# Optimization experiments

Measured on AMD Instinct MI355X. Metric: run time of the kernel, lower is better.

## Reference

```python
import jax, jax.numpy as jnp
import numpy as np

B, S, Lb, C, CP, H = 64, 4, 64, 32, 16, 4
LN_EPS = 1e-5


def layer_norm(x, g, b):
    mu = jnp.mean(x, axis=-1, keepdims=True)
    var = jnp.mean(jnp.square(x - mu), axis=-1, keepdims=True)
    return (x - mu) * jax.lax.rsqrt(var + LN_EPS) * g + b


def mha(x, w_in, b_in, w_out, b_out, h):
    # torch nn.MultiheadAttention, batch_first, self-attention
    Bx, L, Cx = x.shape
    d = Cx // h
    qkv = x @ w_in.T + b_in                      # (Bx, L, 3C)
    q, k, v = jnp.split(qkv, 3, axis=-1)
    sp = lambda t: t.reshape(Bx, L, h, d).transpose(0, 2, 1, 3)  # (Bx,h,L,d)
    q, k, v = sp(q), sp(k), sp(v)
    scale = 1.0 / jnp.sqrt(jnp.asarray(d, x.dtype))
    attn = jax.nn.softmax(jnp.einsum('bhid,bhjd->bhij', q, k) * scale, axis=-1)
    o = jnp.einsum('bhij,bhjd->bhid', attn, v).transpose(0, 2, 1, 3).reshape(Bx, L, Cx)
    return o @ w_out.T + b_out


def setup_inputs() -> dict:
    key = jax.random.key(0)
    ks = jax.random.split(key, 20)
    g = lambda i, shape, s=0.05: (jax.random.normal(ks[i], shape, dtype=jnp.float32) * s)
    inp = {
        'chip_ctcf': jax.random.normal(ks[0], (B, Lb), dtype=jnp.float32),
        'chip_hac':  jax.random.normal(ks[1], (B, Lb), dtype=jnp.float32),
        'chip_me1':  jax.random.normal(ks[2], (B, Lb), dtype=jnp.float32),
        'chip_me3':  jax.random.normal(ks[3], (B, Lb), dtype=jnp.float32),
        'embed_w': g(4, (C, 1)), 'embed_b': g(5, (C,)),
        'pos_embed': g(6, (1, 1, Lb, C), 0.02),
        'row_in_w': g(7, (3 * C, C)), 'row_in_b': g(8, (3 * C,)),
        'row_out_w': g(9, (C, C)), 'row_out_b': g(10, (C,)),
        'row_ln_g': jnp.ones((C,), jnp.float32), 'row_ln_b': jnp.zeros((C,), jnp.float32),
        'col_in_w': g(11, (3 * C, C)), 'col_in_b': g(12, (3 * C,)),
        'col_out_w': g(13, (C, C)), 'col_out_b': g(14, (C,)),
        'col_ln_g': jnp.ones((C,), jnp.float32), 'col_ln_b': jnp.zeros((C,), jnp.float32),
        'proj_w': g(15, (CP, C * C)), 'proj_b': g(16, (CP,)),
        'pln_g': jnp.ones((CP,), jnp.float32), 'pln_b': jnp.zeros((CP,), jnp.float32),
    }
    return inp


def reference(chip_ctcf, chip_hac, chip_me1, chip_me3,
              embed_w, embed_b, pos_embed,
              row_in_w, row_in_b, row_out_w, row_out_b, row_ln_g, row_ln_b,
              col_in_w, col_in_b, col_out_w, col_out_b, col_ln_g, col_ln_b,
              proj_w, proj_b, pln_g, pln_b):
    Bv = chip_ctcf.shape[0]
    signals = jnp.stack([chip_ctcf, chip_hac, chip_me1, chip_me3], axis=1)  # (B,4,64)
    # Linear(1, C): scalar embed
    msa = signals[..., None] * embed_w[:, 0] + embed_b                      # (B,4,64,C)
    msa = msa + pos_embed
    # row attention over the 64 bins, per track
    x = msa.reshape(Bv * S, Lb, C)
    x = layer_norm(x + mha(x, row_in_w, row_in_b, row_out_w, row_out_b, H), row_ln_g, row_ln_b)
    msa = x.reshape(Bv, S, Lb, C)
    # column attention over the 4 tracks, per bin
    x = msa.transpose(0, 2, 1, 3).reshape(Bv * Lb, S, C)
    x = layer_norm(x + mha(x, col_in_w, col_in_b, col_out_w, col_out_b, H), col_ln_g, col_ln_b)
    msa = x.reshape(Bv, Lb, S, C).transpose(0, 2, 1, 3)                     # (B,4,64,C)
    # outer product of the track-mean (as written in the torch source)
    m = jnp.mean(msa, axis=1)                                               # (B,64,C)
    pair = jnp.einsum('bic,bjd->bijcd', m, m).reshape(Bv, Lb, Lb, C * C)    # (B,64,64,1024)
    nrm = jnp.sqrt(jnp.sum(jnp.square(pair), axis=-1, keepdims=True))
    pair = pair / jnp.maximum(nrm, 1e-6)                                    # F.normalize eps=1e-6
    feat = pair @ proj_w.T + proj_b                                         # (B,64,64,CP)
    feat = layer_norm(feat, pln_g, pln_b)
    feat = feat * jax.nn.sigmoid(feat)                                      # SiLU
    return feat.transpose(0, 3, 1, 2)                                       # (B,CP,64,64)
```

## Files before the change

kernel.cpp:

```cpp
#include <hip/hip_runtime.h>
#include <hip/hip_bf16.h>

#define LN_EPS 1e-5f

__global__ __launch_bounds__(256) void k_row(
    const float* __restrict__ ctcf, const float* __restrict__ hac,
    const float* __restrict__ me1,  const float* __restrict__ me3,
    const float* __restrict__ ew,   const float* __restrict__ eb,
    const float* __restrict__ pe,
    const float* __restrict__ w_in, const float* __restrict__ b_in,
    const float* __restrict__ w_out,const float* __restrict__ b_out,
    const float* __restrict__ ln_g, const float* __restrict__ ln_b,
    float* __restrict__ msaR)
{
    __shared__ float sx[64][33];
    __shared__ float sqkv[64 * 100];
    __shared__ float so[64][33];
    __shared__ float swin[96 * 32];
    __shared__ float swout[32 * 32];
    __shared__ float sbin[96];
    __shared__ float sbout[32], sg[32], sb[32];
    __shared__ float smean[64], srstd[64];

    const int blk = blockIdx.x;
    const int s   = blk & 3;
    const int b   = blk >> 2;
    const int tid = threadIdx.x;

    const float* chip = (s == 0) ? ctcf : (s == 1) ? hac : (s == 2) ? me1 : me3;

    for (int n = tid; n < 96 * 32; n += 256) swin[n] = w_in[n];
    for (int n = tid; n < 32 * 32; n += 256) swout[n] = w_out[n];
    if (tid < 96) sbin[tid] = b_in[tid];
    if (tid < 32) {
        sbout[tid] = b_out[tid];
        sg[tid] = ln_g[tid];
        sb[tid] = ln_b[tid];
    }
    for (int n = tid; n < 2048; n += 256) {
        int l = n >> 5, c = n & 31;
        sx[l][c] = chip[b * 64 + l] * ew[c] + eb[c] + pe[l * 32 + c];
    }
    __syncthreads();

    const int l  = tid & 63;
    const int cg = tid >> 6;

    float xr[32];
#pragma unroll
    for (int c = 0; c < 32; ++c) xr[c] = sx[l][c];

#pragma unroll
    for (int i = 0; i < 24; ++i) {
        int cc = i * 4 + cg;
        const float* wr = &swin[cc * 32];
        float acc = sbin[cc];
#pragma unroll
        for (int c = 0; c < 32; ++c) acc += xr[c] * wr[c];
        sqkv[l * 100 + cc] = acc;
    }
    __syncthreads();

    {
        const int h = cg;
        float q[8];
#pragma unroll
        for (int dd = 0; dd < 8; ++dd) q[dd] = sqkv[l * 100 + h * 8 + dd];
        const float scale = 0.35355339059327373f;
        float mrun = -1e30f, denom = 0.f, acc[8];
#pragma unroll
        for (int dd = 0; dd < 8; ++dd) acc[dd] = 0.f;
        for (int j = 0; j < 64; ++j) {
            const float* kr = &sqkv[j * 100 + 32 + h * 8];
            const float* vr = &sqkv[j * 100 + 64 + h * 8];
            float sc = 0.f;
#pragma unroll
            for (int dd = 0; dd < 8; ++dd) sc += q[dd] * kr[dd];
            sc *= scale;
            float mnew = fmaxf(mrun, sc);
            float corr = __expf(mrun - mnew);
            float w = __expf(sc - mnew);
            denom = denom * corr + w;
#pragma unroll
            for (int dd = 0; dd < 8; ++dd)
                acc[dd] = acc[dd] * corr + w * vr[dd];
            mrun = mnew;
        }
        float inv = 1.f / denom;
#pragma unroll
        for (int dd = 0; dd < 8; ++dd) so[l][h * 8 + dd] = acc[dd] * inv;
    }
    __syncthreads();

    {
        float orow[32];
#pragma unroll
        for (int k = 0; k < 32; ++k) orow[k] = so[l][k];
#pragma unroll
        for (int i = 0; i < 8; ++i) {
            int c = i * 4 + cg;
            const float* wr = &swout[c * 32];
            float acc = sbout[c] + xr[c];
#pragma unroll
            for (int k = 0; k < 32; ++k) acc += orow[k] * wr[k];
            sqkv[l * 100 + c] = acc;
        }
    }
    __syncthreads();

    if (tid < 64) {
        float mu = 0.f;
#pragma unroll
        for (int c = 0; c < 32; ++c) mu += sqkv[tid * 100 + c];
        mu *= (1.f / 32.f);
        float var = 0.f;
#pragma unroll
        for (int c = 0; c < 32; ++c) { float d = sqkv[tid * 100 + c] - mu; var += d * d; }
        var *= (1.f / 32.f);
        smean[tid] = mu;
        srstd[tid] = rsqrtf(var + LN_EPS);
    }
    __syncthreads();

    float* outp = msaR + blk * 2048;
    for (int n = tid; n < 2048; n += 256) {
        int ll = n >> 5, c = n & 31;
        outp[n] = (sqkv[ll * 100 + c] - smean[ll]) * srstd[ll] * sg[c] + sb[c];
    }
}

__global__ __launch_bounds__(256) void k_col(
    const float* __restrict__ msaR,
    const float* __restrict__ w_in, const float* __restrict__ b_in,
    const float* __restrict__ w_out,const float* __restrict__ b_out,
    const float* __restrict__ ln_g, const float* __restrict__ ln_b,
    float* __restrict__ m_out, float* __restrict__ nrm_out)
{
    __shared__ float sx[64][33];
    __shared__ float sqkv[64 * 100];
    __shared__ float so[64][33];
    __shared__ float swi[96 * 32];
    __shared__ float swo[32 * 32];
    __shared__ float sbi[96];
    __shared__ float sbo[32], sg[32], sb[32];
    __shared__ float smean2[64], srstd2[64];
    __shared__ float smv[16][33];

    const int bx = blockIdx.x;
    const int b  = bx >> 2;
    const int l0 = (bx & 3) * 16;
    const int tid = threadIdx.x;

    for (int n = tid; n < 96 * 32; n += 256) swi[n] = w_in[n];
    for (int n = tid; n < 32 * 32; n += 256) swo[n] = w_out[n];
    if (tid < 96) sbi[tid] = b_in[tid];
    if (tid < 32) {
        sbo[tid] = b_out[tid];
        sg[tid] = ln_g[tid];
        sb[tid] = ln_b[tid];
    }
    for (int n = tid; n < 2048; n += 256) {
        int s = n >> 9, lo = (n >> 5) & 15, c = n & 31;
        sx[s * 16 + lo][c] = msaR[((b * 4 + s) * 64 + l0 + lo) * 32 + c];
    }
    __syncthreads();

    const int r  = tid & 63;
    const int sS = r & 3, lo = r >> 2;
    const int cg = tid >> 6;

    float xr[32];
#pragma unroll
    for (int c = 0; c < 32; ++c) xr[c] = sx[sS * 16 + lo][c];

#pragma unroll
    for (int i = 0; i < 24; ++i) {
        int cc = i * 4 + cg;
        const float* wr = &swi[cc * 32];
        float acc = sbi[cc];
#pragma unroll
        for (int c = 0; c < 32; ++c) acc += xr[c] * wr[c];
        sqkv[r * 100 + cc] = acc;
    }
    __syncthreads();

    {
        const int la = tid >> 4, h = (tid >> 2) & 3, ia = tid & 3;
        const float scale = 0.35355339059327373f;
        float q[8];
#pragma unroll
        for (int dd = 0; dd < 8; ++dd) q[dd] = sqkv[(la * 4 + ia) * 100 + h * 8 + dd];
        float sc[4];
        float mx = -1e30f;
#pragma unroll
        for (int jj = 0; jj < 4; ++jj) {
            const float* kr = &sqkv[(la * 4 + jj) * 100 + 32 + h * 8];
            float v = 0.f;
#pragma unroll
            for (int dd = 0; dd < 8; ++dd) v += q[dd] * kr[dd];
            sc[jj] = v * scale;
            mx = fmaxf(mx, sc[jj]);
        }
        float den = 0.f;
#pragma unroll
        for (int jj = 0; jj < 4; ++jj) { sc[jj] = __expf(sc[jj] - mx); den += sc[jj]; }
        float inv = 1.f / den;
#pragma unroll
        for (int dd = 0; dd < 8; ++dd) {
            float a = 0.f;
#pragma unroll
            for (int jj = 0; jj < 4; ++jj)
                a += sc[jj] * sqkv[(la * 4 + jj) * 100 + 64 + h * 8 + dd];
            so[la * 4 + ia][h * 8 + dd] = a * inv;
        }
    }
    __syncthreads();

    {
        float orow[32];
#pragma unroll
        for (int k = 0; k < 32; ++k) orow[k] = so[r][k];
#pragma unroll
        for (int i = 0; i < 8; ++i) {
            int c = i * 4 + cg;
            const float* wr = &swo[c * 32];
            float acc = sbo[c] + xr[c];
#pragma unroll
            for (int k = 0; k < 32; ++k) acc += orow[k] * wr[k];
            sqkv[r * 100 + c] = acc;
        }
    }
    __syncthreads();

    if (tid < 64) {
        float mu = 0.f;
#pragma unroll
        for (int c = 0; c < 32; ++c) mu += sqkv[tid * 100 + c];
        mu *= (1.f / 32.f);
        float var = 0.f;
#pragma unroll
        for (int c = 0; c < 32; ++c) { float d = sqkv[tid * 100 + c] - mu; var += d * d; }
        var *= (1.f / 32.f);
        smean2[tid] = mu;
        srstd2[tid] = rsqrtf(var + LN_EPS);
    }
    __syncthreads();

    for (int pass = 0; pass < 2; ++pass) {
        int idx = pass * 256 + tid;
        int loo = idx >> 5, c = idx & 31;
        float acc = 0.f;
#pragma unroll
        for (int ss = 0; ss < 4; ++ss) {
            int rr = loo * 4 + ss;
            acc += (sqkv[rr * 100 + c] - smean2[rr]) * srstd2[rr];
        }
        float mval = 0.25f * acc * sg[c] + sb[c];
        m_out[(b * 64 + l0 + loo) * 32 + c] = mval;
        smv[loo][c] = mval * mval;
    }
    __syncthreads();

    if (tid < 16) {
        float sum = 0.f;
#pragma unroll
        for (int c = 0; c < 32; ++c) sum += smv[tid][c];
        nrm_out[b * 64 + l0 + tid] = sqrtf(sum);
    }
}

__global__ __launch_bounds__(256) void k_pair(
    const float* __restrict__ m, const float* __restrict__ nrm,
    const float* __restrict__ pw, const float* __restrict__ pb,
    const float* __restrict__ pg, const float* __restrict__ pbeta,
    float* __restrict__ out)
{
    __shared__ float spw[512 * 36];
    __shared__ float sT[16 * 520];
    __shared__ float smj[64][33];
    __shared__ float snj[64];
    __shared__ float sbias[16], sgam[16], sbet[16];

    const int bx = blockIdx.x;
    const int b  = bx >> 2;
    const int i0 = (bx & 3) * 16;
    const int tid = threadIdx.x;

    const float* mb = m + b * 2048;
    for (int n = tid; n < 2048; n += 256) smj[n >> 5][n & 31] = mb[n];
    if (tid < 64) snj[tid] = nrm[b * 64 + tid];
    if (tid < 16) {
        sbias[tid] = pb[tid];
        sgam[tid]  = pg[tid];
        sbet[tid]  = pbeta[tid];
    }
    for (int n = tid; n < 16384; n += 256) {
        int cp = n >> 10, c = (n >> 5) & 31, d = n & 31;
        spw[(cp * 32 + d) * 36 + c] = pw[n];
    }
    __syncthreads();

    {
        const int il = tid >> 4, t16 = tid & 15;
        const int ig = i0 + il;
        float mi[32];
#pragma unroll
        for (int c = 0; c < 32; ++c) mi[c] = smj[ig][c];
#pragma unroll
        for (int p = 0; p < 32; ++p) {
            int rem = p * 16 + t16;
            const float* wr = &spw[rem * 36];
            float acc = 0.f;
#pragma unroll
            for (int c = 0; c < 32; ++c) acc += wr[c] * mi[c];
            sT[il * 520 + rem] = acc;
        }
    }
    __syncthreads();

    const int j  = tid & 63;
    const int ih = tid >> 6;
    float mj[32];
#pragma unroll
    for (int d = 0; d < 32; ++d) mj[d] = smj[j][d];
    const float nj = snj[j];

    for (int q = 0; q < 4; ++q) {
        const int il = ih * 4 + q;
        const int ig = i0 + il;
        const float invn = 1.f / fmaxf(snj[ig] * nj, 1e-6f);
        float f[16];
#pragma unroll
        for (int cp = 0; cp < 16; ++cp) {
            const float* tr = &sT[il * 520 + cp * 32];
            float acc = 0.f;
#pragma unroll
            for (int d = 0; d < 32; ++d) acc += tr[d] * mj[d];
            f[cp] = acc * invn + sbias[cp];
        }
        float mu = 0.f;
#pragma unroll
        for (int cp = 0; cp < 16; ++cp) mu += f[cp];
        mu *= (1.f / 16.f);
        float var = 0.f;
#pragma unroll
        for (int cp = 0; cp < 16; ++cp) { float d = f[cp] - mu; var += d * d; }
        var *= (1.f / 16.f);
        const float rstd = rsqrtf(var + LN_EPS);
#pragma unroll
        for (int cp = 0; cp < 16; ++cp) {
            float v = (f[cp] - mu) * rstd * sgam[cp] + sbet[cp];
            float sl = v / (1.f + __expf(-v));
            out[((b * 16 + cp) * 64 + ig) * 64 + j] = sl;
        }
    }
}

extern "C" void kernel_launch(void* const* d_in, const int* in_sizes, int n_in,
                              void* d_out, int out_size, void* d_ws, size_t ws_size,
                              hipStream_t stream) {
    const float* ctcf  = (const float*)d_in[0];
    const float* hac   = (const float*)d_in[1];
    const float* me1   = (const float*)d_in[2];
    const float* me3   = (const float*)d_in[3];
    const float* ew    = (const float*)d_in[4];
    const float* ebias = (const float*)d_in[5];
    const float* pe    = (const float*)d_in[6];
    const float* riw   = (const float*)d_in[7];
    const float* rib   = (const float*)d_in[8];
    const float* row_  = (const float*)d_in[9];
    const float* rob   = (const float*)d_in[10];
    const float* rlg   = (const float*)d_in[11];
    const float* rlb   = (const float*)d_in[12];
    const float* ciw   = (const float*)d_in[13];
    const float* cib   = (const float*)d_in[14];
    const float* cow   = (const float*)d_in[15];
    const float* cob   = (const float*)d_in[16];
    const float* clg   = (const float*)d_in[17];
    const float* clb   = (const float*)d_in[18];
    const float* pw    = (const float*)d_in[19];
    const float* pb    = (const float*)d_in[20];
    const float* pg    = (const float*)d_in[21];
    const float* pbt   = (const float*)d_in[22];

    float* out = (float*)d_out;

    float* msaR = (float*)d_out;
    float* mbuf = (float*)d_ws;
    float* nbuf = mbuf + 64 * 64 * 32;

    k_row<<<256, 256, 0, stream>>>(ctcf, hac, me1, me3, ew, ebias, pe,
                                   riw, rib, row_, rob, rlg, rlb, msaR);
    k_col<<<256, 256, 0, stream>>>(msaR, ciw, cib, cow, cob, clg, clb,
                                   mbuf, nbuf);
    k_pair<<<256, 256, 0, stream>>>(mbuf, nbuf, pw, pb, pg, pbt, out);
}
```

Baseline: 167.2 us.

## Restructure pair-kernel weight staging and T computation with shuffles and vector loads

The proj_w staging loop now reads float4 from global memory and stores into an LDS layout padded to 33 instead of 36. The first contraction is reorganised so each thread owns two weight rows and accumulates all 16 i rows, broadcasting the m_i values through wavefront shuffles. This replaces repeated LDS weight reads with register reuse. The second contraction reads sT with float4 loads, which adds more registers and shuffle traffic in exchange for fewer LDS accesses.

```diff
diff --git a/kernel.cpp b/kernel.cpp
--- a/kernel.cpp
+++ b/kernel.cpp
@@ -275,7 +275,7 @@
     const float* __restrict__ pg, const float* __restrict__ pbeta,
     float* __restrict__ out)
 {
-    __shared__ float spw[512 * 36];
+    __shared__ float spw[512 * 33];
     __shared__ float sT[16 * 520];
     __shared__ float smj[64][33];
     __shared__ float snj[64];
@@ -294,26 +294,48 @@
         sgam[tid]  = pg[tid];
         sbet[tid]  = pbeta[tid];
     }
-    for (int n = tid; n < 16384; n += 256) {
-        int cp = n >> 10, c = (n >> 5) & 31, d = n & 31;
-        spw[(cp * 32 + d) * 36 + c] = pw[n];
-    }
-    __syncthreads();
-
-    {
-        const int il = tid >> 4, t16 = tid & 15;
-        const int ig = i0 + il;
-        float mi[32];
-#pragma unroll
-        for (int c = 0; c < 32; ++c) mi[c] = smj[ig][c];
-#pragma unroll
-        for (int p = 0; p < 32; ++p) {
-            int rem = p * 16 + t16;
-            const float* wr = &spw[rem * 36];
-            float acc = 0.f;
-#pragma unroll
-            for (int c = 0; c < 32; ++c) acc += wr[c] * mi[c];
-            sT[il * 520 + rem] = acc;
+    for (int t = 0; t < 16; ++t) {
+        int n4 = (t * 256 + tid) * 4;
+        float4 wv = *(const float4*)&pw[n4];
+        int cp = n4 >> 10, c = (n4 >> 5) & 31, d = n4 & 31;
+        float* dst = &spw[(cp * 32 + d) * 33 + c];
+        dst[0]      = wv.x;
+        dst[33]     = wv.y;
+        dst[66]     = wv.z;
+        dst[99]     = wv.w;
+    }
+    __syncthreads();
+
+    const int lane = tid & 63;
+    float mi8[8];
+    {
+        const int mil = lane >> 2, mq = lane & 3;
+#pragma unroll
+        for (int k = 0; k < 8; ++k) mi8[k] = smj[i0 + mil][mq * 8 + k];
+    }
+
+    {
+        float acc0[16], acc1[16];
+#pragma unroll
+        for (int il = 0; il < 16; ++il) { acc0[il] = 0.f; acc1[il] = 0.f; }
+        const float* w0p = &spw[tid * 33];
+        const float* w1p = &spw[(tid + 256) * 33];
+#pragma unroll
+        for (int c = 0; c < 32; ++c) {
+            float w0 = w0p[c];
+            float w1 = w1p[c];
+            const int src = c >> 3, k = c & 7;
+#pragma unroll
+            for (int il = 0; il < 16; ++il) {
+                float mval = __shfl(mi8[k], il * 4 + src, 64);
+                acc0[il] += mval * w0;
+                acc1[il] += mval * w1;
+            }
+        }
+#pragma unroll
+        for (int il = 0; il < 16; ++il) {
+            sT[il * 520 + tid]       = acc0[il];
+            sT[il * 520 + tid + 256] = acc1[il];
         }
     }
     __syncthreads();
@@ -332,10 +354,16 @@
         float f[16];
 #pragma unroll
         for (int cp = 0; cp < 16; ++cp) {
-            const float* tr = &sT[il * 520 + cp * 32];
+            const float4* tr = (const float4*)&sT[il * 520 + cp * 32];
             float acc = 0.f;
 #pragma unroll
-            for (int d = 0; d < 32; ++d) acc += tr[d] * mj[d];
+            for (int d4 = 0; d4 < 8; ++d4) {
+                float4 tv = tr[d4];
+                acc += tv.x * mj[d4 * 4 + 0];
+                acc += tv.y * mj[d4 * 4 + 1];
+                acc += tv.z * mj[d4 * 4 + 2];
+                acc += tv.w * mj[d4 * 4 + 3];
+            }
             f[cp] = acc * invn + sbias[cp];
         }
         float mu = 0.f;
```

Result: no change. 167.9 us (+0.4%).

## Compute pair projection from global weights in registers and vectorize LDS reads

Applied to the files above, without the earlier changes.

k_pair no longer stages and transposes the full projection weight matrix into shared memory. Each warp now computes its four T rows in a 4x8 register tile, reading proj_w straight from global memory, and writes only its own rows of sT. That removes one block barrier and cuts shared-memory use sharply, which should allow more resident blocks. Separately, the row and column attention kernels replace scalar LDS loads with float4 loads. The trade-offs are uncoalesced, repeated global reads of the weights (relying on cache) and an intra-warp LDS dependency in place of a barrier.

```diff
diff --git a/kernel.cpp b/kernel.cpp
--- a/kernel.cpp
+++ b/kernel.cpp
@@ -2,6 +2,11 @@
 #include <hip/hip_bf16.h>
 
 #define LN_EPS 1e-5f
+
+__device__ __forceinline__ float dot8(float4 a0, float4 a1, float4 b0, float4 b1) {
+    return a0.x * b0.x + a0.y * b0.y + a0.z * b0.z + a0.w * b0.w +
+           a1.x * b1.x + a1.y * b1.y + a1.z * b1.z + a1.w * b1.w;
+}
 
 __global__ __launch_bounds__(256) void k_row(
     const float* __restrict__ ctcf, const float* __restrict__ hac,
@@ -53,42 +58,45 @@
 #pragma unroll
     for (int i = 0; i < 24; ++i) {
         int cc = i * 4 + cg;
-        const float* wr = &swin[cc * 32];
+        const float4* wr4 = (const float4*)&swin[cc * 32];
         float acc = sbin[cc];
 #pragma unroll
-        for (int c = 0; c < 32; ++c) acc += xr[c] * wr[c];
+        for (int c4 = 0; c4 < 8; ++c4) {
+            float4 wv = wr4[c4];
+            acc += xr[c4 * 4 + 0] * wv.x + xr[c4 * 4 + 1] * wv.y +
+                   xr[c4 * 4 + 2] * wv.z + xr[c4 * 4 + 3] * wv.w;
+        }
         sqkv[l * 100 + cc] = acc;
     }
     __syncthreads();
 
     {
         const int h = cg;
-        float q[8];
-#pragma unroll
-        for (int dd = 0; dd < 8; ++dd) q[dd] = sqkv[l * 100 + h * 8 + dd];
+        const float4* qp = (const float4*)&sqkv[l * 100 + h * 8];
+        float4 q0 = qp[0], q1 = qp[1];
         const float scale = 0.35355339059327373f;
-        float mrun = -1e30f, denom = 0.f, acc[8];
-#pragma unroll
-        for (int dd = 0; dd < 8; ++dd) acc[dd] = 0.f;
+        float mrun = -1e30f, denom = 0.f, a[8];
+#pragma unroll
+        for (int dd = 0; dd < 8; ++dd) a[dd] = 0.f;
         for (int j = 0; j < 64; ++j) {
-            const float* kr = &sqkv[j * 100 + 32 + h * 8];
-            const float* vr = &sqkv[j * 100 + 64 + h * 8];
-            float sc = 0.f;
-#pragma unroll
-            for (int dd = 0; dd < 8; ++dd) sc += q[dd] * kr[dd];
-            sc *= scale;
+            const float4* kp = (const float4*)&sqkv[j * 100 + 32 + h * 8];
+            float4 k0 = kp[0], k1 = kp[1];
+            float sc = dot8(q0, q1, k0, k1) * scale;
+            const float4* vp = (const float4*)&sqkv[j * 100 + 64 + h * 8];
+            float4 v0 = vp[0], v1 = vp[1];
             float mnew = fmaxf(mrun, sc);
             float corr = __expf(mrun - mnew);
             float w = __expf(sc - mnew);
             denom = denom * corr + w;
-#pragma unroll
-            for (int dd = 0; dd < 8; ++dd)
-                acc[dd] = acc[dd] * corr + w * vr[dd];
+            a[0] = a[0] * corr + w * v0.x;  a[1] = a[1] * corr + w * v0.y;
+            a[2] = a[2] * corr + w * v0.z;  a[3] = a[3] * corr + w * v0.w;
+            a[4] = a[4] * corr + w * v1.x;  a[5] = a[5] * corr + w * v1.y;
+            a[6] = a[6] * corr + w * v1.z;  a[7] = a[7] * corr + w * v1.w;
             mrun = mnew;
         }
         float inv = 1.f / denom;
 #pragma unroll
-        for (int dd = 0; dd < 8; ++dd) so[l][h * 8 + dd] = acc[dd] * inv;
+        for (int dd = 0; dd < 8; ++dd) so[l][h * 8 + dd] = a[dd] * inv;
     }
     __syncthreads();
 
@@ -99,10 +107,14 @@
 #pragma unroll
         for (int i = 0; i < 8; ++i) {
             int c = i * 4 + cg;
-            const float* wr = &swout[c * 32];
+            const float4* wr4 = (const float4*)&swout[c * 32];
             float acc = sbout[c] + xr[c];
 #pragma unroll
-            for (int k = 0; k < 32; ++k) acc += orow[k] * wr[k];
+            for (int k4 = 0; k4 < 8; ++k4) {
+                float4 wv = wr4[k4];
+                acc += orow[k4 * 4 + 0] * wv.x + orow[k4 * 4 + 1] * wv.y +
+                       orow[k4 * 4 + 2] * wv.z + orow[k4 * 4 + 3] * wv.w;
+            }
             sqkv[l * 100 + c] = acc;
         }
     }
@@ -176,10 +188,14 @@
 #pragma unroll
     for (int i = 0; i < 24; ++i) {
         int cc = i * 4 + cg;
-        const float* wr = &swi[cc * 32];
+        const float4* wr4 = (const float4*)&swi[cc * 32];
         float acc = sbi[cc];
 #pragma unroll
-        for (int c = 0; c < 32; ++c) acc += xr[c] * wr[c];
+        for (int c4 = 0; c4 < 8; ++c4) {
+            float4 wv = wr4[c4];
+            acc += xr[c4 * 4 + 0] * wv.x + xr[c4 * 4 + 1] * wv.y +
+                   xr[c4 * 4 + 2] * wv.z + xr[c4 * 4 + 3] * wv.w;
+        }
         sqkv[r * 100 + cc] = acc;
     }
     __syncthreads();
@@ -187,32 +203,35 @@
     {
         const int la = tid >> 4, h = (tid >> 2) & 3, ia = tid & 3;
         const float scale = 0.35355339059327373f;
-        float q[8];
-#pragma unroll
-        for (int dd = 0; dd < 8; ++dd) q[dd] = sqkv[(la * 4 + ia) * 100 + h * 8 + dd];
+        const float4* qp = (const float4*)&sqkv[(la * 4 + ia) * 100 + h * 8];
+        float4 q0 = qp[0], q1 = qp[1];
         float sc[4];
         float mx = -1e30f;
 #pragma unroll
         for (int jj = 0; jj < 4; ++jj) {
-            const float* kr = &sqkv[(la * 4 + jj) * 100 + 32 + h * 8];
-            float v = 0.f;
-#pragma unroll
-            for (int dd = 0; dd < 8; ++dd) v += q[dd] * kr[dd];
-            sc[jj] = v * scale;
+            const float4* kp = (const float4*)&sqkv[(la * 4 + jj) * 100 + 32 + h * 8];
+            sc[jj] = dot8(q0, q1, kp[0], kp[1]) * scale;
             mx = fmaxf(mx, sc[jj]);
         }
         float den = 0.f;
 #pragma unroll
         for (int jj = 0; jj < 4; ++jj) { sc[jj] = __expf(sc[jj] - mx); den += sc[jj]; }
         float inv = 1.f / den;
-#pragma unroll
-        for (int dd = 0; dd < 8; ++dd) {
-            float a = 0.f;
-#pragma unroll
-            for (int jj = 0; jj < 4; ++jj)
-                a += sc[jj] * sqkv[(la * 4 + jj) * 100 + 64 + h * 8 + dd];
-            so[la * 4 + ia][h * 8 + dd] = a * inv;
-        }
+        float a[8];
+#pragma unroll
+        for (int dd = 0; dd < 8; ++dd) a[dd] = 0.f;
+#pragma unroll
+        for (int jj = 0; jj < 4; ++jj) {
+            const float4* vp = (const float4*)&sqkv[(la * 4 + jj) * 100 + 64 + h * 8];
+            float4 v0 = vp[0], v1 = vp[1];
+            float wgt = sc[jj];
+            a[0] += wgt * v0.x;  a[1] += wgt * v0.y;
+            a[2] += wgt * v0.z;  a[3] += wgt * v0.w;
+            a[4] += wgt * v1.x;  a[5] += wgt * v1.y;
+            a[6] += wgt * v1.z;  a[7] += wgt * v1.w;
+        }
+#pragma unroll
+        for (int dd = 0; dd < 8; ++dd) so[la * 4 + ia][h * 8 + dd] = a[dd] * inv;
     }
     __syncthreads();
 
@@ -223,10 +242,14 @@
 #pragma unroll
         for (int i = 0; i < 8; ++i) {
             int c = i * 4 + cg;
-            const float* wr = &swo[c * 32];
+            const float4* wr4 = (const float4*)&swo[c * 32];
             float acc = sbo[c] + xr[c];
 #pragma unroll
-            for (int k = 0; k < 32; ++k) acc += orow[k] * wr[k];
+            for (int k4 = 0; k4 < 8; ++k4) {
+                float4 wv = wr4[k4];
+                acc += orow[k4 * 4 + 0] * wv.x + orow[k4 * 4 + 1] * wv.y +
+                       orow[k4 * 4 + 2] * wv.z + orow[k4 * 4 + 3] * wv.w;
+            }
             sqkv[r * 100 + c] = acc;
         }
     }
@@ -275,9 +298,8 @@
     const float* __restrict__ pg, const float* __restrict__ pbeta,
     float* __restrict__ out)
 {
-    __shared__ float spw[512 * 36];
+    __shared__ float smj[64][36];
     __shared__ float sT[16 * 520];
-    __shared__ float smj[64][33];
     __shared__ float snj[64];
     __shared__ float sbias[16], sgam[16], sbet[16];
 
@@ -285,6 +307,7 @@
     const int b  = bx >> 2;
     const int i0 = (bx & 3) * 16;
     const int tid = threadIdx.x;
+    const int lane = tid & 63, w = tid >> 6;
 
     const float* mb = m + b * 2048;
     for (int n = tid; n < 2048; n += 256) smj[n >> 5][n & 31] = mb[n];
@@ -294,48 +317,65 @@
         sgam[tid]  = pg[tid];
         sbet[tid]  = pbeta[tid];
     }
-    for (int n = tid; n < 16384; n += 256) {
-        int cp = n >> 10, c = (n >> 5) & 31, d = n & 31;
-        spw[(cp * 32 + d) * 36 + c] = pw[n];
-    }
-    __syncthreads();
-
-    {
-        const int il = tid >> 4, t16 = tid & 15;
-        const int ig = i0 + il;
-        float mi[32];
-#pragma unroll
-        for (int c = 0; c < 32; ++c) mi[c] = smj[ig][c];
-#pragma unroll
-        for (int p = 0; p < 32; ++p) {
-            int rem = p * 16 + t16;
-            const float* wr = &spw[rem * 36];
-            float acc = 0.f;
-#pragma unroll
-            for (int c = 0; c < 32; ++c) acc += wr[c] * mi[c];
-            sT[il * 520 + rem] = acc;
-        }
-    }
-    __syncthreads();
-
-    const int j  = tid & 63;
-    const int ih = tid >> 6;
+    __syncthreads();
+
+    float treg[4][8];
+#pragma unroll
+    for (int q = 0; q < 4; ++q)
+#pragma unroll
+        for (int k = 0; k < 8; ++k) treg[q][k] = 0.f;
+    {
+        const float* pwl = pw + (lane >> 5) * 1024 + (lane & 31);
+#pragma unroll 4
+        for (int c = 0; c < 32; ++c) {
+            float m0 = smj[i0 + w * 4 + 0][c];
+            float m1 = smj[i0 + w * 4 + 1][c];
+            float m2 = smj[i0 + w * 4 + 2][c];
+            float m3 = smj[i0 + w * 4 + 3][c];
+#pragma unroll
+            for (int k = 0; k < 8; ++k) {
+                float wv = pwl[k * 2048 + c * 32];
+                treg[0][k] += m0 * wv;
+                treg[1][k] += m1 * wv;
+                treg[2][k] += m2 * wv;
+                treg[3][k] += m3 * wv;
+            }
+        }
+    }
+#pragma unroll
+    for (int q = 0; q < 4; ++q)
+#pragma unroll
+        for (int k = 0; k < 8; ++k)
+            sT[(w * 4 + q) * 520 + lane + 64 * k] = treg[q][k];
+
+    const int j = lane;
     float mj[32];
-#pragma unroll
-    for (int d = 0; d < 32; ++d) mj[d] = smj[j][d];
+    {
+        const float4* mjp = (const float4*)&smj[j][0];
+#pragma unroll
+        for (int d4 = 0; d4 < 8; ++d4) {
+            float4 t = mjp[d4];
+            mj[d4 * 4 + 0] = t.x;  mj[d4 * 4 + 1] = t.y;
+            mj[d4 * 4 + 2] = t.z;  mj[d4 * 4 + 3] = t.w;
+        }
+    }
     const float nj = snj[j];
 
     for (int q = 0; q < 4; ++q) {
-        const int il = ih * 4 + q;
+        const int il = w * 4 + q;
         const int ig = i0 + il;
         const float invn = 1.f / fmaxf(snj[ig] * nj, 1e-6f);
         float f[16];
 #pragma unroll
         for (int cp = 0; cp < 16; ++cp) {
-            const float* tr = &sT[il * 520 + cp * 32];
+            const float4* tr = (const float4*)&sT[il * 520 + cp * 32];
             float acc = 0.f;
 #pragma unroll
-            for (int d = 0; d < 32; ++d) acc += tr[d] * mj[d];
+            for (int d4 = 0; d4 < 8; ++d4) {
+                float4 tv = tr[d4];
+                acc += tv.x * mj[d4 * 4 + 0] + tv.y * mj[d4 * 4 + 1] +
+                       tv.z * mj[d4 * 4 + 2] + tv.w * mj[d4 * 4 + 3];
+            }
             f[cp] = acc * invn + sbias[cp];
         }
         float mu = 0.f;
```

After: 164.7 us. Within noise of the previous version (-1.5%).
